# Performance work log

Measured on AMD Instinct MI355X. Metric: run time of the kernel, lower is better.

## Reference

```python
import jax, jax.numpy as jnp
import numpy as np


def _conv_valid(x, w):
    # x: [B, Cin, H, W], w: [Cout, Cin, K, K], stride 1, no padding
    return jax.lax.conv_general_dilated(
        x, w, window_strides=(1, 1), padding='VALID',
        dimension_numbers=('NCHW', 'OIHW', 'NCHW'))


def _buggy_maxpool(x, k=2):
    # Faithful to the source MaxPool: window of size kxk slides with STRIDE 1,
    # but only the first H//k x W//k positions are kept (top-left region).
    nh = x.shape[2] // k
    nw = x.shape[3] // k
    m = jax.lax.reduce_window(
        x, -jnp.inf, jax.lax.max,
        window_dimensions=(1, 1, k, k),
        window_strides=(1, 1, 1, 1),
        padding='VALID')  # [B, C, H-k+1, W-k+1]
    return m[:, :, :nh, :nw]


def setup_inputs() -> dict:
    key = jax.random.key(0)
    ks = jax.random.split(key, 9)
    B = 8192
    x = jax.random.normal(ks[0], (B, 3, 32, 32), dtype=jnp.float32)
    s = 0.1
    conv1_w = jax.random.normal(ks[1], (6, 3, 5, 5), dtype=jnp.float32) * s
    conv2_w = jax.random.normal(ks[2], (16, 6, 5, 5), dtype=jnp.float32) * s
    fc1_w = jax.random.normal(ks[3], (120, 400), dtype=jnp.float32) * s
    fc1_b = jax.random.normal(ks[4], (120,), dtype=jnp.float32) * s
    fc2_w = jax.random.normal(ks[5], (84, 120), dtype=jnp.float32) * s
    fc2_b = jax.random.normal(ks[6], (84,), dtype=jnp.float32) * s
    fc3_w = jax.random.normal(ks[7], (10, 84), dtype=jnp.float32) * s
    fc3_b = jax.random.normal(ks[8], (10,), dtype=jnp.float32) * s
    return {
        'x': x,
        'conv1_w': conv1_w, 'conv2_w': conv2_w,
        'fc1_w': fc1_w, 'fc1_b': fc1_b,
        'fc2_w': fc2_w, 'fc2_b': fc2_b,
        'fc3_w': fc3_w, 'fc3_b': fc3_b,
    }


def reference(x, conv1_w, conv2_w, fc1_w, fc1_b, fc2_w, fc2_b, fc3_w, fc3_b):
    h = _buggy_maxpool(jax.nn.relu(_conv_valid(x, conv1_w)))   # [B,6,14,14]
    h = _buggy_maxpool(jax.nn.relu(_conv_valid(h, conv2_w)))   # [B,16,5,5]
    h = h.reshape(-1, 16 * 5 * 5)                              # [B,400]
    h = jax.nn.relu(h @ fc1_w.T + fc1_b)                       # [B,120]
    h = jax.nn.relu(h @ fc2_w.T + fc2_b)                       # [B,84]
    return h @ fc3_w.T + fc3_b                                 # [B,10]
```

## Files before the change

kernel.cpp:

```cpp
#include <hip/hip_runtime.h>


typedef float v2f __attribute__((ext_vector_type(2)));

__device__ __forceinline__ v2f mk2(float a, float b) { v2f t; t.x = a; t.y = b; return t; }

constexpr int THREADS = 256;
constexpr int IPB = 4;

constexpr int W1_OFF = 0;
constexpr int W2_OFF = 452;
constexpr int IMG_BASE = 2852;
constexpr int XS_OFF = 0;
constexpr int P1_OFF = 0;
constexpr int P2_OFF = 1184;
constexpr int F1_OFF = 0;
constexpr int F2_OFF = 128;
constexpr int IMG_STRIDE = 1600;
constexpr int LDS_FLOATS = IMG_BASE + IPB * IMG_STRIDE;

__device__ __forceinline__ void wave_sync() {
    asm volatile("s_waitcnt lgkmcnt(0)" ::: "memory");
}

extern "C" __global__ __launch_bounds__(THREADS, 4)
void lenet_fused(const float* __restrict__ x,
                 const float* __restrict__ w1,
                 const float* __restrict__ w2,
                 const float* __restrict__ fc1w, const float* __restrict__ fc1b,
                 const float* __restrict__ fc2w, const float* __restrict__ fc2b,
                 const float* __restrict__ fc3w, const float* __restrict__ fc3b,
                 float* __restrict__ out)
{
    __shared__ __align__(16) float lds[LDS_FLOATS];
    const int tid  = threadIdx.x;
    const int lane = tid & 63;
    const int wv   = tid >> 6;
    const int img0 = blockIdx.x * IPB;

    {
        const float4* s1 = (const float4*)w1;
        float4* d1 = (float4*)(lds + W1_OFF);
        for (int i = tid; i < 112; i += THREADS) d1[i] = s1[i];
        if (tid < 2) lds[W1_OFF + 448 + tid] = w1[448 + tid];
        const float4* s2 = (const float4*)w2;
        float4* d2 = (float4*)(lds + W2_OFF);
        for (int i = tid; i < 600; i += THREADS) d2[i] = s2[i];
    }

    float* base = lds + IMG_BASE + wv * IMG_STRIDE;
    {
        const float4* xg = (const float4*)(x + (size_t)(img0 + wv) * 3072);
        float4* xs4 = (float4*)(base + XS_OFF);
        for (int i = lane; i < 285; i += 64) {
            int c = i / 95, rem = i - c * 95;
            int r = rem / 5, c4 = rem - r * 5;
            xs4[i] = xg[c * 256 + r * 8 + c4];
        }
    }
    __syncthreads();

    const float* xs  = base + XS_OFF;
    const float* w1s = lds + W1_OFF;
    float* p1 = base + P1_OFF;
    const v2f zero2 = mk2(0.f, 0.f);

    {
        const int l   = (lane < 45) ? lane : 44;
        const int ocp = l / 15;
        const int r   = l - ocp * 15;
        const int oc0 = ocp * 2;
        v2f acc[15];
        #pragma unroll
        for (int c = 0; c < 15; ++c) acc[c] = zero2;
        for (int ci = 0; ci < 3; ++ci) {
            #pragma unroll
            for (int kr = 0; kr < 5; ++kr) {
                const float* xrow = xs + ci * 380 + (r + kr) * 20;
                float xv[19];
                #pragma unroll
                for (int j = 0; j < 19; ++j) xv[j] = xrow[j];
                const float* wr0 = w1s + oc0 * 75 + ci * 25 + kr * 5;
                #pragma unroll
                for (int kc = 0; kc < 5; ++kc) {
                    const v2f wvv = mk2(wr0[kc], wr0[75 + kc]);
                    #pragma unroll
                    for (int c = 0; c < 15; ++c)
                        acc[c] = __builtin_elementwise_fma(
                            mk2(xv[c + kc], xv[c + kc]), wvv, acc[c]);
                }
            }
        }
        v2f pm[14];
        #pragma unroll
        for (int c = 0; c < 14; ++c)
            pm[c] = __builtin_elementwise_max(
                __builtin_elementwise_max(acc[c], acc[c + 1]), zero2);
        v2f m[14];
        #pragma unroll
        for (int c = 0; c < 14; ++c) {
            m[c].x = fmaxf(pm[c].x, __shfl(pm[c].x, lane + 1, 64));
            m[c].y = fmaxf(pm[c].y, __shfl(pm[c].y, lane + 1, 64));
        }
        wave_sync();
        if (r < 14) {
            float2* d0 = (float2*)(p1 + oc0 * 196 + r * 14);
            float2* d1 = (float2*)(p1 + (oc0 + 1) * 196 + r * 14);
            #pragma unroll
            for (int j = 0; j < 7; ++j) {
                d0[j] = make_float2(m[2 * j].x, m[2 * j + 1].x);
                d1[j] = make_float2(m[2 * j].y, m[2 * j + 1].y);
            }
        }
    }
    wave_sync();

    float* p2 = base + P2_OFF;
    const float* w2s = lds + W2_OFF;
    {
        const int l   = (lane < 48) ? lane : 47;
        const int ocp = l / 6;
        const int r   = l - ocp * 6;
        const int oc0 = ocp * 2;
        v2f acc[6];
        #pragma unroll
        for (int c = 0; c < 6; ++c) acc[c] = zero2;
        for (int ci = 0; ci < 6; ++ci) {
            #pragma unroll
            for (int kr = 0; kr < 5; ++kr) {
                const float* prow = p1 + ci * 196 + (r + kr) * 14;
                float xv[10];
                #pragma unroll
                for (int j = 0; j < 10; ++j) xv[j] = prow[j];
                const float* wr0 = w2s + oc0 * 150 + ci * 25 + kr * 5;
                #pragma unroll
                for (int kc = 0; kc < 5; ++kc) {
                    const v2f wvv = mk2(wr0[kc], wr0[150 + kc]);
                    #pragma unroll
                    for (int c = 0; c < 6; ++c)
                        acc[c] = __builtin_elementwise_fma(
                            mk2(xv[c + kc], xv[c + kc]), wvv, acc[c]);
                }
            }
        }
        v2f pm[5];
        #pragma unroll
        for (int c = 0; c < 5; ++c)
            pm[c] = __builtin_elementwise_max(
                __builtin_elementwise_max(acc[c], acc[c + 1]), zero2);
        v2f m[5];
        #pragma unroll
        for (int c = 0; c < 5; ++c) {
            m[c].x = fmaxf(pm[c].x, __shfl(pm[c].x, lane + 1, 64));
            m[c].y = fmaxf(pm[c].y, __shfl(pm[c].y, lane + 1, 64));
        }
        if (r < 5) {
            float* q0 = p2 + oc0 * 25 + r * 5;
            float* q1 = p2 + (oc0 + 1) * 25 + r * 5;
            #pragma unroll
            for (int c = 0; c < 5; ++c) { q0[c] = m[c].x; q1[c] = m[c].y; }
        }
    }
    __syncthreads();

    float* scr = lds + W2_OFF;
    if (tid < 240) {
        const int row  = tid >> 1;
        const int half = tid & 1;
        const float4* wrow = (const float4*)(fc1w + row * 400) + half * 50;
        const float4* a0p = (const float4*)(lds + IMG_BASE + 0 * IMG_STRIDE + P2_OFF) + half * 50;
        const float4* a1p = (const float4*)(lds + IMG_BASE + 1 * IMG_STRIDE + P2_OFF) + half * 50;
        const float4* a2p = (const float4*)(lds + IMG_BASE + 2 * IMG_STRIDE + P2_OFF) + half * 50;
        const float4* a3p = (const float4*)(lds + IMG_BASE + 3 * IMG_STRIDE + P2_OFF) + half * 50;
        v2f acc0 = zero2, acc1 = zero2, acc2 = zero2, acc3 = zero2;
        #pragma unroll 2
        for (int k = 0; k < 50; ++k) {
            float4 w4 = wrow[k];
            const v2f wxy = mk2(w4.x, w4.y), wzw = mk2(w4.z, w4.w);
            float4 a0 = a0p[k], a1 = a1p[k], a2 = a2p[k], a3 = a3p[k];
            acc0 = __builtin_elementwise_fma(mk2(a0.x, a0.y), wxy, acc0);
            acc0 = __builtin_elementwise_fma(mk2(a0.z, a0.w), wzw, acc0);
            acc1 = __builtin_elementwise_fma(mk2(a1.x, a1.y), wxy, acc1);
            acc1 = __builtin_elementwise_fma(mk2(a1.z, a1.w), wzw, acc1);
            acc2 = __builtin_elementwise_fma(mk2(a2.x, a2.y), wxy, acc2);
            acc2 = __builtin_elementwise_fma(mk2(a2.z, a2.w), wzw, acc2);
            acc3 = __builtin_elementwise_fma(mk2(a3.x, a3.y), wxy, acc3);
            acc3 = __builtin_elementwise_fma(mk2(a3.z, a3.w), wzw, acc3);
        }
        scr[0 * 240 + row * 2 + half] = acc0.x + acc0.y;
        scr[1 * 240 + row * 2 + half] = acc1.x + acc1.y;
        scr[2 * 240 + row * 2 + half] = acc2.x + acc2.y;
        scr[3 * 240 + row * 2 + half] = acc3.x + acc3.y;
    }
    __syncthreads();

    if (tid < 120) {
        const float b = fc1b[tid];
        #pragma unroll
        for (int im = 0; im < 4; ++im) {
            float v = scr[im * 240 + tid * 2] + scr[im * 240 + tid * 2 + 1] + b;
            lds[IMG_BASE + im * IMG_STRIDE + F1_OFF + tid] = fmaxf(v, 0.f);
        }
    }
    __syncthreads();

    if (tid < 84) {
        const int row = tid;
        const float4* wrow = (const float4*)(fc2w + row * 120);
        const float bz = fc2b[row];
        v2f acc0 = zero2, acc1 = zero2, acc2 = zero2, acc3 = zero2;
        const float4* f0 = (const float4*)(lds + IMG_BASE + 0 * IMG_STRIDE + F1_OFF);
        const float4* f1 = (const float4*)(lds + IMG_BASE + 1 * IMG_STRIDE + F1_OFF);
        const float4* f2 = (const float4*)(lds + IMG_BASE + 2 * IMG_STRIDE + F1_OFF);
        const float4* f3 = (const float4*)(lds + IMG_BASE + 3 * IMG_STRIDE + F1_OFF);
        #pragma unroll 2
        for (int k = 0; k < 30; ++k) {
            float4 w4 = wrow[k];
            const v2f wxy = mk2(w4.x, w4.y), wzw = mk2(w4.z, w4.w);
            float4 a0 = f0[k], a1 = f1[k], a2 = f2[k], a3 = f3[k];
            acc0 = __builtin_elementwise_fma(mk2(a0.x, a0.y), wxy, acc0);
            acc0 = __builtin_elementwise_fma(mk2(a0.z, a0.w), wzw, acc0);
            acc1 = __builtin_elementwise_fma(mk2(a1.x, a1.y), wxy, acc1);
            acc1 = __builtin_elementwise_fma(mk2(a1.z, a1.w), wzw, acc1);
            acc2 = __builtin_elementwise_fma(mk2(a2.x, a2.y), wxy, acc2);
            acc2 = __builtin_elementwise_fma(mk2(a2.z, a2.w), wzw, acc2);
            acc3 = __builtin_elementwise_fma(mk2(a3.x, a3.y), wxy, acc3);
            acc3 = __builtin_elementwise_fma(mk2(a3.z, a3.w), wzw, acc3);
        }
        lds[IMG_BASE + 0 * IMG_STRIDE + F2_OFF + row] = fmaxf(acc0.x + acc0.y + bz, 0.f);
        lds[IMG_BASE + 1 * IMG_STRIDE + F2_OFF + row] = fmaxf(acc1.x + acc1.y + bz, 0.f);
        lds[IMG_BASE + 2 * IMG_STRIDE + F2_OFF + row] = fmaxf(acc2.x + acc2.y + bz, 0.f);
        lds[IMG_BASE + 3 * IMG_STRIDE + F2_OFF + row] = fmaxf(acc3.x + acc3.y + bz, 0.f);
    }
    __syncthreads();

    if (tid < 40) {
        const int im  = tid / 10;
        const int row = tid - im * 10;
        const float4* wrow = (const float4*)(fc3w + row * 84);
        const float4* f2 = (const float4*)(lds + IMG_BASE + im * IMG_STRIDE + F2_OFF);
        v2f acc = zero2;
        #pragma unroll
        for (int k = 0; k < 21; ++k) {
            float4 w4 = wrow[k];
            float4 a = f2[k];
            acc = __builtin_elementwise_fma(mk2(a.x, a.y), mk2(w4.x, w4.y), acc);
            acc = __builtin_elementwise_fma(mk2(a.z, a.w), mk2(w4.z, w4.w), acc);
        }
        out[(size_t)(img0 + im) * 10 + row] = acc.x + acc.y + fc3b[row];
    }
}

extern "C" void kernel_launch(void* const* d_in, const int* in_sizes, int n_in,
                              void* d_out, int out_size, void* d_ws, size_t ws_size,
                              hipStream_t stream) {
    const float* x    = (const float*)d_in[0];
    const float* w1   = (const float*)d_in[1];
    const float* w2   = (const float*)d_in[2];
    const float* fc1w = (const float*)d_in[3];
    const float* fc1b = (const float*)d_in[4];
    const float* fc2w = (const float*)d_in[5];
    const float* fc2b = (const float*)d_in[6];
    const float* fc3w = (const float*)d_in[7];
    const float* fc3b = (const float*)d_in[8];
    float* out = (float*)d_out;

    const int B = in_sizes[0] / 3072;
    const int grid = B / IPB;
    lenet_fused<<<grid, THREADS, 0, stream>>>(x, w1, w2, fc1w, fc1b,
                                              fc2w, fc2b, fc3w, fc3b, out);
}
```

Baseline: 239.3 us.

## Compute only the conv outputs consumed by the truncated pools and pipeline LDS loads

Because the buggy maxpool keeps only the top-left region, conv1 now computes 11x11 outputs (instead of 15 rows of 15) and loads only the 15x20 input rows that are needed, shrinking the per-image LDS footprint. Weights are interleaved per output-channel pair at load time so each tap is a single v2f LDS read. Both conv loops are fully unrolled with next-iteration loads of inputs and weights prefetched into registers as float4/float2 vector reads. The fc1 loop unroll rises from 2 to 4. The full unrolling raises register pressure and code size, which may hurt occupancy under the 4-block launch bound.

```diff
diff --git a/kernel.cpp b/kernel.cpp
--- a/kernel.cpp
+++ b/kernel.cpp
@@ -2,21 +2,23 @@
 
 
 typedef float v2f __attribute__((ext_vector_type(2)));
-
 __device__ __forceinline__ v2f mk2(float a, float b) { v2f t; t.x = a; t.y = b; return t; }
+__device__ __forceinline__ v2f shfl2(v2f v, int src) {
+    v2f r; r.x = __shfl(v.x, src, 64); r.y = __shfl(v.y, src, 64); return r;
+}
 
 constexpr int THREADS = 256;
 constexpr int IPB = 4;
 
-constexpr int W1_OFF = 0;
-constexpr int W2_OFF = 452;
+constexpr int W1P_OFF = 0;
+constexpr int W2P_OFF = 452;
 constexpr int IMG_BASE = 2852;
 constexpr int XS_OFF = 0;
 constexpr int P1_OFF = 0;
-constexpr int P2_OFF = 1184;
+constexpr int P2_OFF = 900;
 constexpr int F1_OFF = 0;
 constexpr int F2_OFF = 128;
-constexpr int IMG_STRIDE = 1600;
+constexpr int IMG_STRIDE = 1300;
 constexpr int LDS_FLOATS = IMG_BASE + IPB * IMG_STRIDE;
 
 __device__ __forceinline__ void wave_sync() {
@@ -37,77 +39,92 @@
     const int lane = tid & 63;
     const int wv   = tid >> 6;
     const int img0 = blockIdx.x * IPB;
-
-    {
-        const float4* s1 = (const float4*)w1;
-        float4* d1 = (float4*)(lds + W1_OFF);
-        for (int i = tid; i < 112; i += THREADS) d1[i] = s1[i];
-        if (tid < 2) lds[W1_OFF + 448 + tid] = w1[448 + tid];
-        const float4* s2 = (const float4*)w2;
-        float4* d2 = (float4*)(lds + W2_OFF);
-        for (int i = tid; i < 600; i += THREADS) d2[i] = s2[i];
+    const v2f zero2 = mk2(0.f, 0.f);
+
+    for (int i = tid; i < 450; i += THREADS) {
+        int ocp = i / 150, rem = i - ocp * 150, k = rem >> 1, h = rem & 1;
+        lds[W1P_OFF + i] = w1[(2 * ocp + h) * 75 + k];
+    }
+    for (int i = tid; i < 2400; i += THREADS) {
+        int ocp = i / 300, rem = i - ocp * 300, k = rem >> 1, h = rem & 1;
+        lds[W2P_OFF + i] = w2[(2 * ocp + h) * 150 + k];
     }
 
     float* base = lds + IMG_BASE + wv * IMG_STRIDE;
     {
         const float4* xg = (const float4*)(x + (size_t)(img0 + wv) * 3072);
         float4* xs4 = (float4*)(base + XS_OFF);
-        for (int i = lane; i < 285; i += 64) {
-            int c = i / 95, rem = i - c * 95;
+        for (int i = lane; i < 225; i += 64) {
+            int c = i / 75, rem = i - c * 75;
             int r = rem / 5, c4 = rem - r * 5;
             xs4[i] = xg[c * 256 + r * 8 + c4];
         }
     }
     __syncthreads();
 
-    const float* xs  = base + XS_OFF;
-    const float* w1s = lds + W1_OFF;
     float* p1 = base + P1_OFF;
-    const v2f zero2 = mk2(0.f, 0.f);
 
     {
-        const int l   = (lane < 45) ? lane : 44;
-        const int ocp = l / 15;
-        const int r   = l - ocp * 15;
-        const int oc0 = ocp * 2;
-        v2f acc[15];
-        #pragma unroll
-        for (int c = 0; c < 15; ++c) acc[c] = zero2;
-        for (int ci = 0; ci < 3; ++ci) {
+        const int l   = (lane < 33) ? lane : 32;
+        const int ocp = l / 11;
+        const int r   = l - ocp * 11;
+        const float4* xs4 = (const float4*)(base + XS_OFF);
+        const v2f* w1p = (const v2f*)(lds + W1P_OFF);
+
+        v2f acc[11];
+        #pragma unroll
+        for (int c = 0; c < 11; ++c) acc[c] = zero2;
+
+        float4 Xa = xs4[r * 5 + 0], Xb = xs4[r * 5 + 1],
+               Xc = xs4[r * 5 + 2], Xd = xs4[r * 5 + 3];
+        v2f W0[5];
+        #pragma unroll
+        for (int kc = 0; kc < 5; ++kc) W0[kc] = w1p[ocp * 75 + kc];
+
+        #pragma unroll
+        for (int i = 0; i < 15; ++i) {
+            float4 Na, Nb, Nc, Nd; v2f W1r[5];
+            if (i < 14) {
+                const int ci = (i + 1) / 5, kr = (i + 1) % 5;
+                const int b = ci * 75 + (r + kr) * 5;
+                Na = xs4[b]; Nb = xs4[b + 1]; Nc = xs4[b + 2]; Nd = xs4[b + 3];
+                #pragma unroll
+                for (int kc = 0; kc < 5; ++kc)
+                    W1r[kc] = w1p[ocp * 75 + (i + 1) * 5 + kc];
+            }
+            float xv[16];
+            xv[0]=Xa.x; xv[1]=Xa.y; xv[2]=Xa.z;  xv[3]=Xa.w;
+            xv[4]=Xb.x; xv[5]=Xb.y; xv[6]=Xb.z;  xv[7]=Xb.w;
+            xv[8]=Xc.x; xv[9]=Xc.y; xv[10]=Xc.z; xv[11]=Xc.w;
+            xv[12]=Xd.x; xv[13]=Xd.y; xv[14]=Xd.z; xv[15]=Xd.w;
             #pragma unroll
-            for (int kr = 0; kr < 5; ++kr) {
-                const float* xrow = xs + ci * 380 + (r + kr) * 20;
-                float xv[19];
-                #pragma unroll
-                for (int j = 0; j < 19; ++j) xv[j] = xrow[j];
-                const float* wr0 = w1s + oc0 * 75 + ci * 25 + kr * 5;
-                #pragma unroll
-                for (int kc = 0; kc < 5; ++kc) {
-                    const v2f wvv = mk2(wr0[kc], wr0[75 + kc]);
-                    #pragma unroll
-                    for (int c = 0; c < 15; ++c)
-                        acc[c] = __builtin_elementwise_fma(
-                            mk2(xv[c + kc], xv[c + kc]), wvv, acc[c]);
-                }
-            }
-        }
-        v2f pm[14];
-        #pragma unroll
-        for (int c = 0; c < 14; ++c)
-            pm[c] = __builtin_elementwise_max(
-                __builtin_elementwise_max(acc[c], acc[c + 1]), zero2);
-        v2f m[14];
-        #pragma unroll
-        for (int c = 0; c < 14; ++c) {
-            m[c].x = fmaxf(pm[c].x, __shfl(pm[c].x, lane + 1, 64));
-            m[c].y = fmaxf(pm[c].y, __shfl(pm[c].y, lane + 1, 64));
-        }
+            for (int kc = 0; kc < 5; ++kc)
+                #pragma unroll
+                for (int c = 0; c < 11; ++c)
+                    acc[c] = __builtin_elementwise_fma(
+                        mk2(xv[c + kc], xv[c + kc]), W0[kc], acc[c]);
+            if (i < 14) {
+                Xa = Na; Xb = Nb; Xc = Nc; Xd = Nd;
+                #pragma unroll
+                for (int kc = 0; kc < 5; ++kc) W0[kc] = W1r[kc];
+            }
+        }
+
+        v2f a[11], pm[10], m[10];
+        #pragma unroll
+        for (int c = 0; c < 11; ++c) a[c] = __builtin_elementwise_max(acc[c], zero2);
+        #pragma unroll
+        for (int c = 0; c < 10; ++c) pm[c] = __builtin_elementwise_max(a[c], a[c + 1]);
+        #pragma unroll
+        for (int c = 0; c < 10; ++c)
+            m[c] = __builtin_elementwise_max(pm[c], shfl2(pm[c], lane + 1));
         wave_sync();
-        if (r < 14) {
-            float2* d0 = (float2*)(p1 + oc0 * 196 + r * 14);
-            float2* d1 = (float2*)(p1 + (oc0 + 1) * 196 + r * 14);
+        if (r < 10) {
+            const int oc0 = ocp * 2;
+            float2* d0 = (float2*)(p1 + oc0 * 120 + r * 12);
+            float2* d1 = (float2*)(p1 + (oc0 + 1) * 120 + r * 12);
             #pragma unroll
-            for (int j = 0; j < 7; ++j) {
+            for (int j = 0; j < 5; ++j) {
                 d0[j] = make_float2(m[2 * j].x, m[2 * j + 1].x);
                 d1[j] = make_float2(m[2 * j].y, m[2 * j + 1].y);
             }
@@ -116,54 +133,73 @@
     wave_sync();
 
     float* p2 = base + P2_OFF;
-    const float* w2s = lds + W2_OFF;
     {
         const int l   = (lane < 48) ? lane : 47;
         const int ocp = l / 6;
         const int r   = l - ocp * 6;
-        const int oc0 = ocp * 2;
+        const float4* p14 = (const float4*)p1;
+        const float2* p12 = (const float2*)p1;
+        const v2f* w2p = (const v2f*)(lds + W2P_OFF);
+
         v2f acc[6];
         #pragma unroll
         for (int c = 0; c < 6; ++c) acc[c] = zero2;
-        for (int ci = 0; ci < 6; ++ci) {
+
+        float4 Xa = p14[r * 3 + 0], Xb = p14[r * 3 + 1];
+        float2 Xc = p12[r * 6 + 4];
+        v2f W0[5];
+        #pragma unroll
+        for (int kc = 0; kc < 5; ++kc) W0[kc] = w2p[ocp * 150 + kc];
+
+        #pragma unroll
+        for (int i = 0; i < 30; ++i) {
+            float4 Na, Nb; float2 Nc; v2f W1r[5];
+            if (i < 29) {
+                const int ci = (i + 1) / 5, kr = (i + 1) % 5;
+                Na = p14[ci * 30 + (r + kr) * 3 + 0];
+                Nb = p14[ci * 30 + (r + kr) * 3 + 1];
+                Nc = p12[ci * 60 + (r + kr) * 6 + 4];
+                #pragma unroll
+                for (int kc = 0; kc < 5; ++kc)
+                    W1r[kc] = w2p[ocp * 150 + (i + 1) * 5 + kc];
+            }
+            float xv[10];
+            xv[0]=Xa.x; xv[1]=Xa.y; xv[2]=Xa.z; xv[3]=Xa.w;
+            xv[4]=Xb.x; xv[5]=Xb.y; xv[6]=Xb.z; xv[7]=Xb.w;
+            xv[8]=Xc.x; xv[9]=Xc.y;
             #pragma unroll
-            for (int kr = 0; kr < 5; ++kr) {
-                const float* prow = p1 + ci * 196 + (r + kr) * 14;
-                float xv[10];
-                #pragma unroll
-                for (int j = 0; j < 10; ++j) xv[j] = prow[j];
-                const float* wr0 = w2s + oc0 * 150 + ci * 25 + kr * 5;
-                #pragma unroll
-                for (int kc = 0; kc < 5; ++kc) {
-                    const v2f wvv = mk2(wr0[kc], wr0[150 + kc]);
-                    #pragma unroll
-                    for (int c = 0; c < 6; ++c)
-                        acc[c] = __builtin_elementwise_fma(
-                            mk2(xv[c + kc], xv[c + kc]), wvv, acc[c]);
-                }
-            }
-        }
-        v2f pm[5];
+            for (int kc = 0; kc < 5; ++kc)
+                #pragma unroll
+                for (int c = 0; c < 6; ++c)
+                    acc[c] = __builtin_elementwise_fma(
+                        mk2(xv[c + kc], xv[c + kc]), W0[kc], acc[c]);
+            if (i < 29) {
+                Xa = Na; Xb = Nb; Xc = Nc;
+                #pragma unroll
+                for (int kc = 0; kc < 5; ++kc) W0[kc] = W1r[kc];
+            }
+        }
+
+        v2f a[6], pm[5], m[5];
+        #pragma unroll
+        for (int c = 0; c < 6; ++c) a[c] = __builtin_elementwise_max(acc[c], zero2);
+        #pragma unroll
+        for (int c = 0; c < 5; ++c) pm[c] = __builtin_elementwise_max(a[c], a[c + 1]);
         #pragma unroll
         for (int c = 0; c < 5; ++c)
-            pm[c] = __builtin_elementwise_max(
-                __builtin_elementwise_max(acc[c], acc[c + 1]), zero2);
-        v2f m[5];
-        #pragma unroll
-        for (int c = 0; c < 5; ++c) {
-            m[c].x = fmaxf(pm[c].x, __shfl(pm[c].x, lane + 1, 64));
-            m[c].y = fmaxf(pm[c].y, __shfl(pm[c].y, lane + 1, 64));
-        }
+            m[c] = __builtin_elementwise_max(pm[c], shfl2(pm[c], lane + 1));
         if (r < 5) {
-            float* q0 = p2 + oc0 * 25 + r * 5;
-            float* q1 = p2 + (oc0 + 1) * 25 + r * 5;
+            const int oc0 = ocp * 2;
             #pragma unroll
-            for (int c = 0; c < 5; ++c) { q0[c] = m[c].x; q1[c] = m[c].y; }
-        }
-    }
-    __syncthreads();
-
-    float* scr = lds + W2_OFF;
+            for (int c = 0; c < 5; ++c) {
+                p2[oc0 * 25 + r * 5 + c]       = m[c].x;
+                p2[(oc0 + 1) * 25 + r * 5 + c] = m[c].y;
+            }
+        }
+    }
+    __syncthreads();
+
+    float* scr = lds + W2P_OFF;
     if (tid < 240) {
         const int row  = tid >> 1;
         const int half = tid & 1;
@@ -173,7 +209,7 @@
         const float4* a2p = (const float4*)(lds + IMG_BASE + 2 * IMG_STRIDE + P2_OFF) + half * 50;
         const float4* a3p = (const float4*)(lds + IMG_BASE + 3 * IMG_STRIDE + P2_OFF) + half * 50;
         v2f acc0 = zero2, acc1 = zero2, acc2 = zero2, acc3 = zero2;
-        #pragma unroll 2
+        #pragma unroll 4
         for (int k = 0; k < 50; ++k) {
             float4 w4 = wrow[k];
             const v2f wxy = mk2(w4.x, w4.y), wzw = mk2(w4.z, w4.w);
```

Result: no change. 234.7 us (-1.9%).
